# Optimization experiments

Measured on AMD Instinct MI355X. Metric: run time of the kernel, lower is better.

Reference implementation:

```python
import jax, jax.numpy as jnp
import numpy as np

N, E, IN, D, H, G = 10000, 320000, 256, 128, 4, 64


def setup_inputs() -> dict:
    key = jax.random.key(0)
    ks = jax.random.split(key, 16)
    s = 0.05
    x = jax.random.normal(ks[0], (N, IN), jnp.float32)
    W1s = jax.random.normal(ks[1], (IN, H * D), jnp.float32) * s
    b1s = jnp.zeros((H * D,), jnp.float32)
    W1d = jax.random.normal(ks[2], (IN, H * D), jnp.float32) * s
    b1d = jnp.zeros((H * D,), jnp.float32)
    attn1 = jax.random.normal(ks[3], (H, D), jnp.float32) * s
    W2s = jax.random.normal(ks[4], (H * D, D), jnp.float32) * s
    b2s = jnp.zeros((D,), jnp.float32)
    W2d = jax.random.normal(ks[5], (H * D, D), jnp.float32) * s
    b2d = jnp.zeros((D,), jnp.float32)
    attn2 = jax.random.normal(ks[6], (1, D), jnp.float32) * s
    Wr1 = jax.random.normal(ks[7], (D, 64), jnp.float32) * s
    br1 = jnp.zeros((64,), jnp.float32)
    Wr2 = jax.random.normal(ks[8], (64, 1), jnp.float32) * s
    br2 = jnp.zeros((1,), jnp.float32)
    src = jax.random.randint(ks[9], (E,), 0, N)
    dst = jax.random.randint(ks[10], (E,), 0, N)
    # batched-graph node->graph assignment (contiguous, like dgl.batch)
    graph_ids = (jnp.arange(N) * G) // N
    return dict(x=x, W1s=W1s, b1s=b1s, W1d=W1d, b1d=b1d, attn1=attn1,
                W2s=W2s, b2s=b2s, W2d=W2d, b2d=b2d, attn2=attn2,
                Wr1=Wr1, br1=br1, Wr2=Wr2, br2=br2,
                src=src, dst=dst, graph_ids=graph_ids, num_graphs=G)


def gatv2_layer(x, Ws, bs, Wd, bd, attn, src, dst, n):
    """DGL GATv2Conv: e = a . leaky_relu(W_s x_u + W_d x_v), softmax over dst."""
    heads = attn.shape[0]
    hs = (x @ Ws + bs).reshape(n, heads, -1)   # [N,H,D] source projection
    hd = (x @ Wd + bd).reshape(n, heads, -1)   # [N,H,D] dest projection
    e = jax.nn.leaky_relu(hs[src] + hd[dst], negative_slope=0.2)  # [E,H,D]
    score = jnp.einsum('ehd,hd->eh', e, attn)  # [E,H]
    m = jax.ops.segment_max(score, dst, num_segments=n)           # [N,H]
    ex = jnp.exp(score - m[dst])
    denom = jax.ops.segment_sum(ex, dst, num_segments=n)
    alpha = ex / denom[dst]                                       # [E,H]
    out = jax.ops.segment_sum(alpha[:, :, None] * hs[src], dst, num_segments=n)
    return out  # [N,H,D]


def reference(x, W1s, b1s, W1d, b1d, attn1, W2s, b2s, W2d, b2d, attn2,
              Wr1, br1, Wr2, br2, src, dst, graph_ids, num_graphs):
    n = x.shape[0]
    h = gatv2_layer(x, W1s, b1s, W1d, b1d, attn1, src, dst, n).reshape(n, -1)  # [N,H*D]
    h = gatv2_layer(h, W2s, b2s, W2d, b2d, attn2, src, dst, n).mean(axis=1)    # [N,D]
    counts = jax.ops.segment_sum(jnp.ones((n,), h.dtype), graph_ids, num_segments=num_graphs)
    hg = jax.ops.segment_sum(h, graph_ids, num_segments=num_graphs) / jnp.maximum(counts, 1.0)[:, None]
    out = jax.nn.relu(hg @ Wr1 + br1) @ Wr2 + br2  # [G,1]
    return out.squeeze(-1)
```

## Files before the change

kernel.cpp:

```cpp
#include <hip/hip_runtime.h>

typedef __attribute__((ext_vector_type(8))) short bf16x8;
typedef __attribute__((ext_vector_type(4))) float f32x4;

#define N_NODES 10000
#define N_EDGES 320000
#define DIM_IN  256
#define DD      128
#define HH      4
#define HD      512
#define GG      64

__global__ void hist_kernel(const int* __restrict__ dst, int* __restrict__ cnt) {
  int e = blockIdx.x * 256 + threadIdx.x;
  atomicAdd(&cnt[dst[e]], 1);
}

__global__ void scan_kernel(const int* __restrict__ cnt, int* __restrict__ row_off) {
  __shared__ int part[1024];
  int t = threadIdx.x;
  int base = t * 10;
  int s = 0;
#pragma unroll
  for (int i = 0; i < 10; i++) { int idx = base + i; if (idx < N_NODES) s += cnt[idx]; }
  part[t] = s;
  __syncthreads();
  for (int off = 1; off < 1024; off <<= 1) {
    int v = (t >= off) ? part[t - off] : 0;
    __syncthreads();
    part[t] += v;
    __syncthreads();
  }
  int run = part[t] - s;
  for (int i = 0; i < 10; i++) {
    int idx = base + i;
    if (idx < N_NODES) { row_off[idx] = run; run += cnt[idx]; }
  }
  if (t == 1023) row_off[N_NODES] = part[1023];
}

__global__ void scatter_kernel(const int* __restrict__ src, const int* __restrict__ dst,
                               const int* __restrict__ row_off,
                               int* __restrict__ fill, int* __restrict__ srcl) {
  int e = blockIdx.x * 256 + threadIdx.x;
  int d = dst[e];
  int pos = row_off[d] + atomicAdd(&fill[d], 1);
  srcl[pos] = src[e];
}

__device__ inline void split4(float4 v, ushort4& h, ushort4& l) {
  uint bx = __float_as_uint(v.x), by = __float_as_uint(v.y);
  uint bz = __float_as_uint(v.z), bw = __float_as_uint(v.w);
  float rx = v.x - __uint_as_float(bx & 0xFFFF0000u);
  float ry = v.y - __uint_as_float(by & 0xFFFF0000u);
  float rz = v.z - __uint_as_float(bz & 0xFFFF0000u);
  float rw = v.w - __uint_as_float(bw & 0xFFFF0000u);
  h.x = (unsigned short)(bx >> 16); h.y = (unsigned short)(by >> 16);
  h.z = (unsigned short)(bz >> 16); h.w = (unsigned short)(bw >> 16);
  l.x = (unsigned short)(__float_as_uint(rx) >> 16);
  l.y = (unsigned short)(__float_as_uint(ry) >> 16);
  l.z = (unsigned short)(__float_as_uint(rz) >> 16);
  l.w = (unsigned short)(__float_as_uint(rw) >> 16);
}

__global__ __launch_bounds__(256) void split_rm(const float* __restrict__ in,
                                                ushort* __restrict__ oh,
                                                ushort* __restrict__ ol, int n4) {
  int i = blockIdx.x * 256 + threadIdx.x;
  if (i >= n4) return;
  float4 v = ((const float4*)in)[i];
  ushort4 h, l;
  split4(v, h, l);
  ((ushort4*)oh)[i] = h;
  ((ushort4*)ol)[i] = l;
}

__global__ __launch_bounds__(256) void split_tr2(
    const float* __restrict__ in0, ushort* __restrict__ oh0, ushort* __restrict__ ol0,
    const float* __restrict__ in1, ushort* __restrict__ oh1, ushort* __restrict__ ol1,
    int K, int N, int lgN) {
  const float* in = blockIdx.y ? in1 : in0;
  ushort* oh = blockIdx.y ? oh1 : oh0;
  ushort* ol = blockIdx.y ? ol1 : ol0;
  int id = blockIdx.x * 256 + threadIdx.x;
  int n = id & (N - 1);
  int kq = id >> lgN;
  if (kq >= (K >> 2)) return;
  int k = kq * 4;
  float4 v;
  v.x = in[(size_t)(k + 0) * N + n];
  v.y = in[(size_t)(k + 1) * N + n];
  v.z = in[(size_t)(k + 2) * N + n];
  v.w = in[(size_t)(k + 3) * N + n];
  ushort4 h, l;
  split4(v, h, l);
  *(ushort4*)(oh + (size_t)n * K + k) = h;
  *(ushort4*)(ol + (size_t)n * K + k) = l;
}

template <int K, int NCOL>
__global__ __launch_bounds__(256) void dual_gemm_mfma(
    const ushort* __restrict__ Ahg, const ushort* __restrict__ Alg,
    const ushort* __restrict__ B1hg, const ushort* __restrict__ B1lg,
    const float* __restrict__ bias1,
    const ushort* __restrict__ B2hg, const ushort* __restrict__ B2lg,
    const float* __restrict__ bias2,
    float* __restrict__ C1, float* __restrict__ C2, int M) {
  __shared__ ushort Ah[64][40], Al[64][40];
  __shared__ ushort B1h[64][40], B1l[64][40], B2h[64][40], B2l[64][40];
  int t = threadIdx.x;
  int lane = t & 63, wv = t >> 6;
  int wr = wv >> 1, wc = wv & 1;
  int l15 = lane & 15, l16 = lane >> 4;
  int col0 = blockIdx.x * 64, m0 = blockIdx.y * 64;

  int sr = t >> 2;
  int sk = (t & 3) * 8;
  bool arow_ok = (m0 + sr) < M;
  const ushort* pAh = Ahg + (size_t)(m0 + sr) * K + sk;
  const ushort* pAl = Alg + (size_t)(m0 + sr) * K + sk;
  const ushort* pB1h = B1hg + (size_t)(col0 + sr) * K + sk;
  const ushort* pB1l = B1lg + (size_t)(col0 + sr) * K + sk;
  const ushort* pB2h = B2hg + (size_t)(col0 + sr) * K + sk;
  const ushort* pB2l = B2lg + (size_t)(col0 + sr) * K + sk;

  f32x4 zero = {0.f, 0.f, 0.f, 0.f};
  f32x4 acc1[2][2], acc2[2][2];
#pragma unroll
  for (int i = 0; i < 2; i++)
#pragma unroll
    for (int j = 0; j < 2; j++) { acc1[i][j] = zero; acc2[i][j] = zero; }

  uint4 vah, val, v1h, v1l, v2h, v2l;
#define LOADK(KO)                                                            \
  vah = arow_ok ? *(const uint4*)(pAh + (KO)) : make_uint4(0u, 0u, 0u, 0u);  \
  val = arow_ok ? *(const uint4*)(pAl + (KO)) : make_uint4(0u, 0u, 0u, 0u);  \
  v1h = *(const uint4*)(pB1h + (KO));                                        \
  v1l = *(const uint4*)(pB1l + (KO));                                        \
  v2h = *(const uint4*)(pB2h + (KO));                                        \
  v2l = *(const uint4*)(pB2l + (KO));
  LOADK(0)
  for (int k0 = 0; k0 < K; k0 += 32) {
    __syncthreads();
    *(uint4*)&Ah[sr][sk] = vah;
    *(uint4*)&Al[sr][sk] = val;
    *(uint4*)&B1h[sr][sk] = v1h;
    *(uint4*)&B1l[sr][sk] = v1l;
    *(uint4*)&B2h[sr][sk] = v2h;
    *(uint4*)&B2l[sr][sk] = v2l;
    __syncthreads();
    if (k0 + 32 < K) { LOADK(k0 + 32) }
#pragma unroll
    for (int cb = 0; cb < 2; cb++) {
      int bc = wc * 32 + cb * 16 + l15;
      bf16x8 b1hf = *(const bf16x8*)&B1h[bc][l16 * 8];
      bf16x8 b1lf = *(const bf16x8*)&B1l[bc][l16 * 8];
      bf16x8 b2hf = *(const bf16x8*)&B2h[bc][l16 * 8];
      bf16x8 b2lf = *(const bf16x8*)&B2l[bc][l16 * 8];
#pragma unroll
      for (int rb = 0; rb < 2; rb++) {
        int arw = wr * 32 + rb * 16 + l15;
        bf16x8 ahf = *(const bf16x8*)&Ah[arw][l16 * 8];
        bf16x8 alf = *(const bf16x8*)&Al[arw][l16 * 8];
        acc1[rb][cb] = __builtin_amdgcn_mfma_f32_16x16x32_bf16(ahf, b1hf, acc1[rb][cb], 0, 0, 0);
        acc1[rb][cb] = __builtin_amdgcn_mfma_f32_16x16x32_bf16(ahf, b1lf, acc1[rb][cb], 0, 0, 0);
        acc1[rb][cb] = __builtin_amdgcn_mfma_f32_16x16x32_bf16(alf, b1hf, acc1[rb][cb], 0, 0, 0);
        acc2[rb][cb] = __builtin_amdgcn_mfma_f32_16x16x32_bf16(ahf, b2hf, acc2[rb][cb], 0, 0, 0);
        acc2[rb][cb] = __builtin_amdgcn_mfma_f32_16x16x32_bf16(ahf, b2lf, acc2[rb][cb], 0, 0, 0);
        acc2[rb][cb] = __builtin_amdgcn_mfma_f32_16x16x32_bf16(alf, b2hf, acc2[rb][cb], 0, 0, 0);
      }
    }
  }
#undef LOADK
#pragma unroll
  for (int rb = 0; rb < 2; rb++) {
#pragma unroll
    for (int cb = 0; cb < 2; cb++) {
      int row = m0 + wr * 32 + rb * 16 + l16 * 4;
      int col = col0 + wc * 32 + cb * 16 + l15;
      float bb1 = bias1[col], bb2 = bias2[col];
#pragma unroll
      for (int rr = 0; rr < 4; rr++) {
        if (row + rr < M) {
          C1[(size_t)(row + rr) * NCOL + col] = acc1[rb][cb][rr] + bb1;
          C2[(size_t)(row + rr) * NCOL + col] = acc2[rb][cb][rr] + bb2;
        }
      }
    }
  }
}

__global__ __launch_bounds__(64) void fused_gat1(
    const float* __restrict__ hs, const float* __restrict__ hd,
    const float* __restrict__ attn, const int* __restrict__ row_off,
    const int* __restrict__ srcl,
    ushort* __restrict__ outh, ushort* __restrict__ outl) {
  int lane = threadIdx.x;
  int slice = blockIdx.x & 3;
  int v = blockIdx.x >> 2;
  int grp = lane >> 4, sl = lane & 15;
  int off = slice * 128 + sl * 8;
  int start = row_off[v];
  int deg = row_off[v + 1] - start;

  const float* ap = attn + off;
  const float* hp = hd + (size_t)v * HD + off;
  float4 a0 = *(const float4*)ap, a1 = *(const float4*)(ap + 4);
  float4 g0 = *(const float4*)hp, g1 = *(const float4*)(hp + 4);
  float areg[8] = {a0.x, a0.y, a0.z, a0.w, a1.x, a1.y, a1.z, a1.w};
  float hdreg[8] = {g0.x, g0.y, g0.z, g0.w, g1.x, g1.y, g1.z, g1.w};
  float a6[8], a4[8];
#pragma unroll
  for (int j = 0; j < 8; j++) { a6[j] = 0.6f * areg[j]; a4[j] = 0.4f * areg[j]; }
  const float* hsl = hs + off;

  float ssum = 0.f;
  float acc[8] = {0.f, 0.f, 0.f, 0.f, 0.f, 0.f, 0.f, 0.f};

  for (int base = 0; base < deg; base += 64) {
    int nc = deg - base; nc = nc < 64 ? nc : 64;
    int myidx = (lane < nc) ? srcl[start + base + lane] : 0;

    float4 cAa = {0,0,0,0}, cAb = {0,0,0,0}, cBa = {0,0,0,0}, cBb = {0,0,0,0};
    {
      int eA = grp, eB = grp + 4;
      int idxA = __shfl(myidx, eA < nc ? eA : 0);
      int idxB = __shfl(myidx, eB < nc ? eB : 0);
      if (eA < nc) { const float* p = hsl + (size_t)idxA * HD; cAa = *(const float4*)p; cAb = *(const float4*)(p + 4); }
      if (eB < nc) { const float* p = hsl + (size_t)idxB * HD; cBa = *(const float4*)p; cBb = *(const float4*)(p + 4); }
    }

    for (int i0 = 0; i0 < nc; i0 += 8) {
#define GAT1_STEP(S, CA, CB)                                                   \
      { int e = i0 + 4 * S + grp;                                              \
        int nx = i0 + 8 + 4 * S + grp;                                         \
        int nidx = __shfl(myidx, nx < nc ? nx : 0);    \
        bool vld = e < nc;                                                     \
        float u[8] = {CA.x, CA.y, CA.z, CA.w, CB.x, CB.y, CB.z, CB.w};         \
        if (nx < nc) {                                                         \
          const float* p = hsl + (size_t)nidx * HD;                            \
          CA = *(const float4*)p; CB = *(const float4*)(p + 4);                \
        }                                                                      \
        float part = 0.f;                                                      \
        _Pragma("unroll")                                                      \
        for (int j = 0; j < 8; j++) {                                          \
          float ee = u[j] + hdreg[j];                                          \
          part = fmaf(ee, a6[j], part);                                        \
          part = fmaf(fabsf(ee), a4[j], part);                                 \
        }                                                                      \
        _Pragma("unroll")                                                      \
        for (int k = 1; k < 16; k <<= 1) part += __shfl_xor(part, k);          \
        float wg = vld ? __expf(part) : 0.f;                                   \
        ssum += wg;                                                            \
        _Pragma("unroll")                                                      \
        for (int j = 0; j < 8; j++) acc[j] = fmaf(wg, u[j], acc[j]);           \
      }
      GAT1_STEP(0, cAa, cAb)
      GAT1_STEP(1, cBa, cBb)
#undef GAT1_STEP
    }
  }
#pragma unroll
  for (int j = 0; j < 8; j++) {
    acc[j] += __shfl_xor(acc[j], 16);
    acc[j] += __shfl_xor(acc[j], 32);
  }
  ssum += __shfl_xor(ssum, 16);
  ssum += __shfl_xor(ssum, 32);
  if (lane < 16) {
    float inv = ssum > 0.f ? 1.f / ssum : 0.f;
    float4 o0 = make_float4(acc[0] * inv, acc[1] * inv, acc[2] * inv, acc[3] * inv);
    float4 o1 = make_float4(acc[4] * inv, acc[5] * inv, acc[6] * inv, acc[7] * inv);
    ushort4 hv0, lv0, hv1, lv1;
    split4(o0, hv0, lv0);
    split4(o1, hv1, lv1);
    *(ushort4*)(outh + (size_t)v * HD + off) = hv0;
    *(ushort4*)(outh + (size_t)v * HD + off + 4) = hv1;
    *(ushort4*)(outl + (size_t)v * HD + off) = lv0;
    *(ushort4*)(outl + (size_t)v * HD + off + 4) = lv1;
  }
}

__global__ __launch_bounds__(64) void fused_gat2(
    const float* __restrict__ hs, const float* __restrict__ hd,
    const float* __restrict__ attn, const int* __restrict__ row_off,
    const int* __restrict__ srcl, float* __restrict__ out) {
  int lane = threadIdx.x, grp = lane >> 4, sl = lane & 15;
  int v = blockIdx.x;
  int start = row_off[v];
  int deg = row_off[v + 1] - start;

  const float* ap = attn + sl * 8;
  const float* hp = hd + (size_t)v * DD + sl * 8;
  float4 a0 = *(const float4*)ap, a1 = *(const float4*)(ap + 4);
  float4 g0 = *(const float4*)hp, g1 = *(const float4*)(hp + 4);
  float areg[8] = {a0.x, a0.y, a0.z, a0.w, a1.x, a1.y, a1.z, a1.w};
  float hdreg[8] = {g0.x, g0.y, g0.z, g0.w, g1.x, g1.y, g1.z, g1.w};
  float a6[8], a4[8];
#pragma unroll
  for (int j = 0; j < 8; j++) { a6[j] = 0.6f * areg[j]; a4[j] = 0.4f * areg[j]; }
  const float* hsl = hs + sl * 8;

  float ssum = 0.f;
  float acc[8] = {0.f, 0.f, 0.f, 0.f, 0.f, 0.f, 0.f, 0.f};

  float4 c0a = {0,0,0,0}, c0b = {0,0,0,0}, c1a = {0,0,0,0}, c1b = {0,0,0,0};
  if (grp < deg) { const float* p = hsl + (size_t)srcl[start + grp] * DD; c0a = *(const float4*)p; c0b = *(const float4*)(p + 4); }
  if (grp + 4 < deg) { const float* p = hsl + (size_t)srcl[start + grp + 4] * DD; c1a = *(const float4*)p; c1b = *(const float4*)(p + 4); }

  for (int i = grp; i < deg; i += 8) {
    float u0[8] = {c0a.x, c0a.y, c0a.z, c0a.w, c0b.x, c0b.y, c0b.z, c0b.w};
    float u1[8] = {c1a.x, c1a.y, c1a.z, c1a.w, c1b.x, c1b.y, c1b.z, c1b.w};
    bool have1 = (i + 4) < deg;
    if (i + 8 < deg) { const float* p = hsl + (size_t)srcl[start + i + 8] * DD; c0a = *(const float4*)p; c0b = *(const float4*)(p + 4); }
    if (i + 12 < deg) { const float* p = hsl + (size_t)srcl[start + i + 12] * DD; c1a = *(const float4*)p; c1b = *(const float4*)(p + 4); }
    float part0 = 0.f, part1 = 0.f;
#pragma unroll
    for (int j = 0; j < 8; j++) {
      float e0 = u0[j] + hdreg[j];
      part0 = fmaf(e0, a6[j], part0);
      part0 = fmaf(fabsf(e0), a4[j], part0);
      float e1 = u1[j] + hdreg[j];
      part1 = fmaf(e1, a6[j], part1);
      part1 = fmaf(fabsf(e1), a4[j], part1);
    }
#pragma unroll
    for (int k = 1; k < 16; k <<= 1) {
      part0 += __shfl_xor(part0, k);
      part1 += __shfl_xor(part1, k);
    }
    float wg0 = __expf(part0);
    float wg1 = have1 ? __expf(part1) : 0.f;
    ssum += wg0 + wg1;
#pragma unroll
    for (int j = 0; j < 8; j++)
      acc[j] = fmaf(wg0, u0[j], fmaf(wg1, u1[j], acc[j]));
  }
#pragma unroll
  for (int j = 0; j < 8; j++) {
    acc[j] += __shfl_xor(acc[j], 16);
    acc[j] += __shfl_xor(acc[j], 32);
  }
  ssum += __shfl_xor(ssum, 16);
  ssum += __shfl_xor(ssum, 32);
  float inv = ssum > 0.f ? 1.f / ssum : 0.f;
  if (lane < 16) {
    float* op = out + (size_t)v * DD + sl * 8;
    *(float4*)op = make_float4(acc[0] * inv, acc[1] * inv, acc[2] * inv, acc[3] * inv);
    *(float4*)(op + 4) = make_float4(acc[4] * inv, acc[5] * inv, acc[6] * inv, acc[7] * inv);
  }
}

__global__ __launch_bounds__(128) void final_kernel(
    const float* __restrict__ h2, const int* __restrict__ gid,
    const float* __restrict__ Wr1, const float* __restrict__ br1,
    const float* __restrict__ Wr2, const float* __restrict__ br2,
    float* __restrict__ out) {
  int g = blockIdx.x, t = threadIdx.x;
  int a, b;
  { int l = 0, h = N_NODES; while (l < h) { int m = (l + h) >> 1; if (gid[m] < g) l = m + 1; else h = m; } a = l; }
  { int l = a, h = N_NODES; while (l < h) { int m = (l + h) >> 1; if (gid[m] < g + 1) l = m + 1; else h = m; } b = l; }
  float s0 = 0.f, s1 = 0.f, s2 = 0.f, s3 = 0.f;
  int v = a;
  for (; v + 3 < b; v += 4) {
    s0 += h2[(size_t)(v + 0) * DD + t];
    s1 += h2[(size_t)(v + 1) * DD + t];
    s2 += h2[(size_t)(v + 2) * DD + t];
    s3 += h2[(size_t)(v + 3) * DD + t];
  }
  for (; v < b; v++) s0 += h2[(size_t)v * DD + t];
  __shared__ float hgn[128];
  float cnt = (float)(b - a);
  hgn[t] = ((s0 + s1) + (s2 + s3)) / fmaxf(cnt, 1.f);
  __syncthreads();
  if (t < 64) {
    float r = br1[t];
#pragma unroll 8
    for (int k = 0; k < 128; k++) r = fmaf(hgn[k], Wr1[k * 64 + t], r);
    r = fmaxf(r, 0.f);
    float p = r * Wr2[t];
#pragma unroll
    for (int k = 1; k < 64; k <<= 1) p += __shfl_xor(p, k);
    if (t == 0) out[g] = p + br2[0];
  }
}

extern "C" void kernel_launch(void* const* d_in, const int* in_sizes, int n_in,
                              void* d_out, int out_size, void* d_ws, size_t ws_size,
                              hipStream_t stream) {
  (void)in_sizes; (void)n_in; (void)out_size; (void)ws_size;
  const float* x     = (const float*)d_in[0];
  const float* W1s   = (const float*)d_in[1];
  const float* b1s   = (const float*)d_in[2];
  const float* W1d   = (const float*)d_in[3];
  const float* b1d   = (const float*)d_in[4];
  const float* attn1 = (const float*)d_in[5];
  const float* W2s   = (const float*)d_in[6];
  const float* b2s   = (const float*)d_in[7];
  const float* W2d   = (const float*)d_in[8];
  const float* b2d   = (const float*)d_in[9];
  const float* attn2 = (const float*)d_in[10];
  const float* Wr1   = (const float*)d_in[11];
  const float* br1   = (const float*)d_in[12];
  const float* Wr2   = (const float*)d_in[13];
  const float* br2   = (const float*)d_in[14];
  const int* src     = (const int*)d_in[15];
  const int* dst     = (const int*)d_in[16];
  const int* gid     = (const int*)d_in[17];
  float* out = (float*)d_out;

  char* ws = (char*)d_ws;
  float*  hs1     = (float*)(ws + 0);
  float*  hd1     = (float*)(ws + 20480000);
  ushort* h1h     = (ushort*)(ws + 40960000);
  ushort* h1l     = (ushort*)(ws + 51200000);
  ushort* xh      = (ushort*)(ws + 61440000);
  ushort* xl      = (ushort*)(ws + 66560000);
  int*    srcl    = (int*)(ws + 71680000);
  int*    row_off = (int*)(ws + 72960000);
  int*    cnt     = (int*)(ws + 73000064);
  int*    fill    = (int*)(ws + 73040064);
  ushort* b1sh    = (ushort*)(ws + 73080064);
  ushort* b1sl    = (ushort*)(ws + 73342208);
  ushort* b1dh    = (ushort*)(ws + 73604352);
  ushort* b1dl    = (ushort*)(ws + 73866496);
  ushort* b2sh    = (ushort*)(ws + 74128640);
  ushort* b2sl    = (ushort*)(ws + 74259712);
  ushort* b2dh    = (ushort*)(ws + 74390784);
  ushort* b2dl    = (ushort*)(ws + 74521856);
  float*  hs2     = (float*)(ws + 0);
  float*  hd2     = (float*)(ws + 5120000);
  float*  h2      = (float*)(ws + 40960000);

  hipMemsetAsync(cnt, 0, 2 * N_NODES * 4, stream);

  hist_kernel<<<N_EDGES / 256, 256, 0, stream>>>(dst, cnt);
  scan_kernel<<<1, 1024, 0, stream>>>(cnt, row_off);
  scatter_kernel<<<N_EDGES / 256, 256, 0, stream>>>(src, dst, row_off, fill, srcl);

  split_rm<<<(N_NODES * DIM_IN / 4 + 255) / 256, 256, 0, stream>>>(x, xh, xl, N_NODES * DIM_IN / 4);
  split_tr2<<<dim3((HD * (DIM_IN / 4) + 255) / 256, 2), 256, 0, stream>>>(
      W1s, b1sh, b1sl, W1d, b1dh, b1dl, DIM_IN, HD, 9);
  split_tr2<<<dim3((DD * (HD / 4) + 255) / 256, 2), 256, 0, stream>>>(
      W2s, b2sh, b2sl, W2d, b2dh, b2dl, HD, DD, 7);

  dual_gemm_mfma<DIM_IN, HD><<<dim3(HD / 64, (N_NODES + 63) / 64), 256, 0, stream>>>(
      xh, xl, b1sh, b1sl, b1s, b1dh, b1dl, b1d, hs1, hd1, N_NODES);
  fused_gat1<<<4 * N_NODES, 64, 0, stream>>>(hs1, hd1, attn1, row_off, srcl, h1h, h1l);

  dual_gemm_mfma<HD, DD><<<dim3(DD / 64, (N_NODES + 63) / 64), 256, 0, stream>>>(
      h1h, h1l, b2sh, b2sl, b2s, b2dh, b2dl, b2d, hs2, hd2, N_NODES);
  fused_gat2<<<N_NODES, 64, 0, stream>>>(hs2, hd2, attn2, row_off, srcl, h2);

  final_kernel<<<GG, 128, 0, stream>>>(h2, gid, Wr1, br1, Wr2, br2, out);
}
```

Measured before the change: 206.1 us.

## Use packed f32 math in GAT kernels and split layer-1 aggregation by head pairs

```diff
diff --git a/kernel.cpp b/kernel.cpp
--- a/kernel.cpp
+++ b/kernel.cpp
@@ -2,6 +2,7 @@
 
 typedef __attribute__((ext_vector_type(8))) short bf16x8;
 typedef __attribute__((ext_vector_type(4))) float f32x4;
+typedef __attribute__((ext_vector_type(2))) float f32x2;
 
 #define N_NODES 10000
 #define N_EDGES 320000
@@ -10,6 +11,15 @@
 #define HH      4
 #define HD      512
 #define GG      64
+
+__device__ inline f32x2 pk_add(f32x2 a, f32x2 b) {
+  f32x2 d;
+  asm("v_pk_add_f32 %0, %1, %2" : "=v"(d) : "v"(a), "v"(b));
+  return d;
+}
+__device__ inline void pk_fma_acc(f32x2& acc, f32x2 a, f32x2 b) {
+  asm("v_pk_fma_f32 %0, %1, %2, %0" : "+v"(acc) : "v"(a), "v"(b));
+}
 
 __global__ void hist_kernel(const int* __restrict__ dst, int* __restrict__ cnt) {
   int e = blockIdx.x * 256 + threadIdx.x;
@@ -194,10 +204,10 @@
     const float* __restrict__ hs, const float* __restrict__ hd,
     const float* __restrict__ attn, const int* __restrict__ row_off,
     const int* __restrict__ srcl,
-    ushort* __restrict__ outh, ushort* __restrict__ outl) {
+    ushort* __restrict__ outh, ushort* __restrict__ outl, int slice_base) {
   int lane = threadIdx.x;
-  int slice = blockIdx.x & 3;
-  int v = blockIdx.x >> 2;
+  int slice = slice_base + (blockIdx.x & 1);
+  int v = blockIdx.x >> 1;
   int grp = lane >> 4, sl = lane & 15;
   int off = slice * 128 + sl * 8;
   int start = row_off[v];
@@ -208,14 +218,14 @@
   float4 a0 = *(const float4*)ap, a1 = *(const float4*)(ap + 4);
   float4 g0 = *(const float4*)hp, g1 = *(const float4*)(hp + 4);
   float areg[8] = {a0.x, a0.y, a0.z, a0.w, a1.x, a1.y, a1.z, a1.w};
-  float hdreg[8] = {g0.x, g0.y, g0.z, g0.w, g1.x, g1.y, g1.z, g1.w};
   float a6[8], a4[8];
 #pragma unroll
   for (int j = 0; j < 8; j++) { a6[j] = 0.6f * areg[j]; a4[j] = 0.4f * areg[j]; }
+  f32x2 hd2[4] = {{g0.x, g0.y}, {g0.z, g0.w}, {g1.x, g1.y}, {g1.z, g1.w}};
   const float* hsl = hs + off;
 
   float ssum = 0.f;
-  float acc[8] = {0.f, 0.f, 0.f, 0.f, 0.f, 0.f, 0.f, 0.f};
+  f32x2 acc2[4] = {{0.f, 0.f}, {0.f, 0.f}, {0.f, 0.f}, {0.f, 0.f}};
 
   for (int base = 0; base < deg; base += 64) {
     int nc = deg - base; nc = nc < 64 ? nc : 64;
@@ -236,41 +246,53 @@
         int nx = i0 + 8 + 4 * S + grp;                                         \
         int nidx = __shfl(myidx, nx < nc ? nx : 0);    \
         bool vld = e < nc;                                                     \
-        float u[8] = {CA.x, CA.y, CA.z, CA.w, CB.x, CB.y, CB.z, CB.w};         \
+        f32x2 u0 = {CA.x, CA.y}, u1 = {CA.z, CA.w};                            \
+        f32x2 u2 = {CB.x, CB.y}, u3 = {CB.z, CB.w};                            \
         if (nx < nc) {                                                         \
           const float* p = hsl + (size_t)nidx * HD;                            \
           CA = *(const float4*)p; CB = *(const float4*)(p + 4);                \
         }                                                                      \
+        f32x2 e0 = pk_add(u0, hd2[0]);                                         \
+        f32x2 e1 = pk_add(u1, hd2[1]);                                         \
+        f32x2 e2 = pk_add(u2, hd2[2]);                                         \
+        f32x2 e3 = pk_add(u3, hd2[3]);                                         \
         float part = 0.f;                                                      \
-        _Pragma("unroll")                                                      \
-        for (int j = 0; j < 8; j++) {                                          \
-          float ee = u[j] + hdreg[j];                                          \
-          part = fmaf(ee, a6[j], part);                                        \
-          part = fmaf(fabsf(ee), a4[j], part);                                 \
-        }                                                                      \
+        part = fmaf(e0.x, a6[0], part); part = fmaf(fabsf(e0.x), a4[0], part); \
+        part = fmaf(e0.y, a6[1], part); part = fmaf(fabsf(e0.y), a4[1], part); \
+        part = fmaf(e1.x, a6[2], part); part = fmaf(fabsf(e1.x), a4[2], part); \
+        part = fmaf(e1.y, a6[3], part); part = fmaf(fabsf(e1.y), a4[3], part); \
+        part = fmaf(e2.x, a6[4], part); part = fmaf(fabsf(e2.x), a4[4], part); \
+        part = fmaf(e2.y, a6[5], part); part = fmaf(fabsf(e2.y), a4[5], part); \
+        part = fmaf(e3.x, a6[6], part); part = fmaf(fabsf(e3.x), a4[6], part); \
+        part = fmaf(e3.y, a6[7], part); part = fmaf(fabsf(e3.y), a4[7], part); \
         _Pragma("unroll")                                                      \
         for (int k = 1; k < 16; k <<= 1) part += __shfl_xor(part, k);          \
         float wg = vld ? __expf(part) : 0.f;                                   \
         ssum += wg;                                                            \
-        _Pragma("unroll")                                                      \
-        for (int j = 0; j < 8; j++) acc[j] = fmaf(wg, u[j], acc[j]);           \
+        f32x2 wg2 = {wg, wg};                                                  \
+        pk_fma_acc(acc2[0], wg2, u0);                                          \
+        pk_fma_acc(acc2[1], wg2, u1);                                          \
+        pk_fma_acc(acc2[2], wg2, u2);                                          \
+        pk_fma_acc(acc2[3], wg2, u3);                                          \
       }
       GAT1_STEP(0, cAa, cAb)
       GAT1_STEP(1, cBa, cBb)
 #undef GAT1_STEP
     }
   }
+  float accf[8] = {acc2[0].x, acc2[0].y, acc2[1].x, acc2[1].y,
+                   acc2[2].x, acc2[2].y, acc2[3].x, acc2[3].y};
 #pragma unroll
   for (int j = 0; j < 8; j++) {
-    acc[j] += __shfl_xor(acc[j], 16);
-    acc[j] += __shfl_xor(acc[j], 32);
+    accf[j] += __shfl_xor(accf[j], 16);
+    accf[j] += __shfl_xor(accf[j], 32);
   }
   ssum += __shfl_xor(ssum, 16);
   ssum += __shfl_xor(ssum, 32);
   if (lane < 16) {
     float inv = ssum > 0.f ? 1.f / ssum : 0.f;
-    float4 o0 = make_float4(acc[0] * inv, acc[1] * inv, acc[2] * inv, acc[3] * inv);
-    float4 o1 = make_float4(acc[4] * inv, acc[5] * inv, acc[6] * inv, acc[7] * inv);
+    float4 o0 = make_float4(accf[0] * inv, accf[1] * inv, accf[2] * inv, accf[3] * inv);
+    float4 o1 = make_float4(accf[4] * inv, accf[5] * inv, accf[6] * inv, accf[7] * inv);
     ushort4 hv0, lv0, hv1, lv1;
     split4(o0, hv0, lv0);
     split4(o1, hv1, lv1);
@@ -295,59 +317,69 @@
   float4 a0 = *(const float4*)ap, a1 = *(const float4*)(ap + 4);
   float4 g0 = *(const float4*)hp, g1 = *(const float4*)(hp + 4);
   float areg[8] = {a0.x, a0.y, a0.z, a0.w, a1.x, a1.y, a1.z, a1.w};
-  float hdreg[8] = {g0.x, g0.y, g0.z, g0.w, g1.x, g1.y, g1.z, g1.w};
   float a6[8], a4[8];
 #pragma unroll
   for (int j = 0; j < 8; j++) { a6[j] = 0.6f * areg[j]; a4[j] = 0.4f * areg[j]; }
+  f32x2 hd2[4] = {{g0.x, g0.y}, {g0.z, g0.w}, {g1.x, g1.y}, {g1.z, g1.w}};
   const float* hsl = hs + sl * 8;
 
   float ssum = 0.f;
-  float acc[8] = {0.f, 0.f, 0.f, 0.f, 0.f, 0.f, 0.f, 0.f};
+  f32x2 acc2[4] = {{0.f, 0.f}, {0.f, 0.f}, {0.f, 0.f}, {0.f, 0.f}};
 
   float4 c0a = {0,0,0,0}, c0b = {0,0,0,0}, c1a = {0,0,0,0}, c1b = {0,0,0,0};
   if (grp < deg) { const float* p = hsl + (size_t)srcl[start + grp] * DD; c0a = *(const float4*)p; c0b = *(const float4*)(p + 4); }
   if (grp + 4 < deg) { const float* p = hsl + (size_t)srcl[start + grp + 4] * DD; c1a = *(const float4*)p; c1b = *(const float4*)(p + 4); }
 
   for (int i = grp; i < deg; i += 8) {
-    float u0[8] = {c0a.x, c0a.y, c0a.z, c0a.w, c0b.x, c0b.y, c0b.z, c0b.w};
-    float u1[8] = {c1a.x, c1a.y, c1a.z, c1a.w, c1b.x, c1b.y, c1b.z, c1b.w};
-    bool have1 = (i + 4) < deg;
-    if (i + 8 < deg) { const float* p = hsl + (size_t)srcl[start + i + 8] * DD; c0a = *(const float4*)p; c0b = *(const float4*)(p + 4); }
-    if (i + 12 < deg) { const float* p = hsl + (size_t)srcl[start + i + 12] * DD; c1a = *(const float4*)p; c1b = *(const float4*)(p + 4); }
-    float part0 = 0.f, part1 = 0.f;
-#pragma unroll
-    for (int j = 0; j < 8; j++) {
-      float e0 = u0[j] + hdreg[j];
-      part0 = fmaf(e0, a6[j], part0);
-      part0 = fmaf(fabsf(e0), a4[j], part0);
-      float e1 = u1[j] + hdreg[j];
-      part1 = fmaf(e1, a6[j], part1);
-      part1 = fmaf(fabsf(e1), a4[j], part1);
+#define GAT2_STEP(COND, NEXTI, CA, CB)                                         \
+    { bool vld = (COND);                                                       \
+      f32x2 u0 = {CA.x, CA.y}, u1 = {CA.z, CA.w};                              \
+      f32x2 u2 = {CB.x, CB.y}, u3 = {CB.z, CB.w};                              \
+      if ((NEXTI) < deg) {                                                     \
+        const float* p = hsl + (size_t)srcl[start + (NEXTI)] * DD;             \
+        CA = *(const float4*)p; CB = *(const float4*)(p + 4);                  \
+      }                                                                        \
+      f32x2 e0 = pk_add(u0, hd2[0]);                                           \
+      f32x2 e1 = pk_add(u1, hd2[1]);                                           \
+      f32x2 e2 = pk_add(u2, hd2[2]);                                           \
+      f32x2 e3 = pk_add(u3, hd2[3]);                                           \
+      float part = 0.f;                                                        \
+      part = fmaf(e0.x, a6[0], part); part = fmaf(fabsf(e0.x), a4[0], part);   \
+      part = fmaf(e0.y, a6[1], part); part = fmaf(fabsf(e0.y), a4[1], part);   \
+      part = fmaf(e1.x, a6[2], part); part = fmaf(fabsf(e1.x), a4[2], part);   \
+      part = fmaf(e1.y, a6[3], part); part = fmaf(fabsf(e1.y), a4[3], part);   \
+      part = fmaf(e2.x, a6[4], part); part = fmaf(fabsf(e2.x), a4[4], part);   \
+      part = fmaf(e2.y, a6[5], part); part = fmaf(fabsf(e2.y), a4[5], part);   \
+      part = fmaf(e3.x, a6[6], part); part = fmaf(fabsf(e3.x), a4[6], part);   \
+      part = fmaf(e3.y, a6[7], part); part = fmaf(fabsf(e3.y), a4[7], part);   \
+      _Pragma("unroll")                                                        \
+      for (int k = 1; k < 16; k <<= 1) part += __shfl_xor(part, k);            \
+      float wg = vld ? __expf(part) : 0.f;                                     \
+      ssum += wg;                                                              \
+      f32x2 wg2 = {wg, wg};                                                    \
+      pk_fma_acc(acc2[0], wg2, u0);                                            \
+      pk_fma_acc(acc2[1], wg2, u1);                                            \
+      pk_fma_acc(acc2[2], wg2, u2);                                            \
+      pk_fma_acc(acc2[3], wg2, u3);                                            \
     }
-#pragma unroll
-    for (int k = 1; k < 16; k <<= 1) {
-      part0 += __shfl_xor(part0, k);
-      part1 += __shfl_xor(part1, k);
-    }
-    float wg0 = __expf(part0);
-    float wg1 = have1 ? __expf(part1) : 0.f;
-    ssum += wg0 + wg1;
-#pragma unroll
-    for (int j = 0; j < 8; j++)
-      acc[j] = fmaf(wg0, u0[j], fmaf(wg1, u1[j], acc[j]));
-  }
+    GAT2_STEP(true, i + 8, c0a, c0b)
+    GAT2_STEP((i + 4) < deg, i + 12, c1a, c1b)
+#undef GAT2_STEP
+  }
+  float accf[8] = {acc2[0].x, acc2[0].y, acc2[1].x, acc2[1].y,
+                   acc2[2].x, acc2[2].y, acc2[3].x, acc2[3].y};
 #pragma unroll
   for (int j = 0; j < 8; j++) {
-    acc[j] += __shfl_xor(acc[j], 16);
-    acc[j] += __shfl_xor(acc[j], 32);
+    accf[j] += __shfl_xor(accf[j], 16);
+    accf[j] += __shfl_xor(accf[j], 32);
   }
   ssum += __shfl_xor(ssum, 16);
   ssum += __shfl_xor(ssum, 32);
   float inv = ssum > 0.f ? 1.f / ssum : 0.f;
   if (lane < 16) {
     float* op = out + (size_t)v * DD + sl * 8;
-    *(float4*)op = make_float4(acc[0] * inv, acc[1] * inv, acc[2] * inv, acc[3] * inv);
-    *(float4*)(op + 4) = make_float4(acc[4] * inv, acc[5] * inv, acc[6] * inv, acc[7] * inv);
+    *(float4*)op = make_float4(accf[0] * inv, accf[1] * inv, accf[2] * inv, accf[3] * inv);
+    *(float4*)(op + 4) = make_float4(accf[4] * inv, accf[5] * inv, accf[6] * inv, accf[7] * inv);
   }
 }
 
@@ -446,7 +478,8 @@
 
   dual_gemm_mfma<DIM_IN, HD><<<dim3(HD / 64, (N_NODES + 63) / 64), 256, 0, stream>>>(
       xh, xl, b1sh, b1sl, b1s, b1dh, b1dl, b1d, hs1, hd1, N_NODES);
-  fused_gat1<<<4 * N_NODES, 64, 0, stream>>>(hs1, hd1, attn1, row_off, srcl, h1h, h1l);
+  fused_gat1<<<2 * N_NODES, 64, 0, stream>>>(hs1, hd1, attn1, row_off, srcl, h1h, h1l, 0);
+  fused_gat1<<<2 * N_NODES, 64, 0, stream>>>(hs1, hd1, attn1, row_off, srcl, h1h, h1l, 2);
 
   dual_gemm_mfma<HD, DD><<<dim3(DD / 64, (N_NODES + 63) / 64), 256, 0, stream>>>(
       h1h, h1l, b2sh, b2sl, b2s, b2dh, b2dl, b2d, hs2, hd2, N_NODES);
```

Measured after the change: 215.5 us. 4.6% more time.
